# Optimization experiments

Hardware: AMD Instinct MI355X
Metric: run time of the kernel (lower is better)

The kernel has to match this reference:

```python
import jax, jax.numpy as jnp
import numpy as np

SEQ, B, CIN, H, K = 2048, 16, 512, 512, 2

def setup_inputs() -> dict:
    key = jax.random.key(0)
    k1, k2, k3 = jax.random.split(key, 3)
    x = jax.random.normal(k1, (SEQ, B, CIN), dtype=jnp.float32)
    W = jax.random.normal(k2, (3 * H, CIN, K), dtype=jnp.float32) * (1.0 / np.sqrt(CIN * K))
    b = jax.random.normal(k3, (3 * H,), dtype=jnp.float32) * 0.01
    return {"x": x, "W": W, "b": b}

def _qrnn_fo(x, W, b):
    # x: (T, B, Cin) -> conv input (B, Cin, T), causal left pad of K-1 zeros
    xb = jnp.transpose(x, (1, 2, 0))
    g = jax.lax.conv_general_dilated(
        xb, W, window_strides=(1,), padding=[(K - 1, 0)],
        dimension_numbers=("NCH", "OIH", "NCH"))
    g = g + b[None, :, None]
    g = jnp.transpose(g, (2, 0, 1))  # (T, B, 3H)
    zg, fg, og = jnp.split(g, 3, axis=-1)
    z = jnp.tanh(zg)
    f = jax.nn.sigmoid(fg)
    o = jax.nn.sigmoid(og)

    def step(c, gates_t):
        zt, ft, ot = gates_t
        c = ft * c + (1.0 - ft) * zt
        h = c * ot
        return c, h

    c0 = jnp.zeros((B, H), dtype=x.dtype)
    c_last, hs = jax.lax.scan(step, c0, (z, f, o))
    return hs, c_last

def reference(x, W, b):
    hs, c_last = _qrnn_fo(x, W, b)
    h_last = hs[-1]
    return hs, h_last[None, :], c_last[None, :]
```

## Files before the change

kernel.cpp:

```cpp
#include <hip/hip_runtime.h>

#define SEQ   2048
#define BATCH 16
#define CINCH 512
#define HDIM  512
#define NDIM  1536
#define TBM   (SEQ*BATCH)
#define KRED  1024
#define NCH   128
#define CHL   16
#define NCOL  8192

typedef unsigned short ushort_t;
typedef __bf16 bf16x8 __attribute__((ext_vector_type(8)));
typedef unsigned short u16x8 __attribute__((ext_vector_type(8)));
typedef float f32x4 __attribute__((ext_vector_type(4)));

__device__ __forceinline__ float bf2f(ushort_t u) {
    return __uint_as_float(((unsigned int)u) << 16);
}
__device__ __forceinline__ ushort_t f2bf(float x) {
    unsigned int u = __float_as_uint(x);
    unsigned int r = u + 0x7fffu + ((u >> 16) & 1u);
    return (ushort_t)(r >> 16);
}

#define CAST_BLK 8196
#define RPK_BLK  6144
__global__ void prep_kernel(const float* __restrict__ x, ushort_t* __restrict__ xb,
                            const float* __restrict__ W, ushort_t* __restrict__ wb) {
    if (blockIdx.x < CAST_BLK) {
        int e = (blockIdx.x * 256 + threadIdx.x) * 8;
        u16x8 r;
        if (e < BATCH * CINCH) {
            r = (u16x8){0, 0, 0, 0, 0, 0, 0, 0};
        } else {
            const float* p = x + (e - BATCH * CINCH);
            float4 v0 = *(const float4*)p;
            float4 v1 = *(const float4*)(p + 4);
            r[0] = f2bf(v0.x); r[1] = f2bf(v0.y); r[2] = f2bf(v0.z); r[3] = f2bf(v0.w);
            r[4] = f2bf(v1.x); r[5] = f2bf(v1.y); r[6] = f2bf(v1.z); r[7] = f2bf(v1.w);
        }
        *(u16x8*)(xb + e) = r;
    } else {
        int i = (blockIdx.x - CAST_BLK) * 256 + threadIdx.x;
        int o  = i >> 10;
        int r  = i & 1023;
        int k  = r >> 9;
        int ci = r & 511;
        wb[i] = f2bf(W[o * 1024 + ci * 2 + k]);
    }
}

__device__ __forceinline__ void load_lds_16B(const ushort_t* g, ushort_t* l) {
    auto* gp = reinterpret_cast<const __attribute__((address_space(1))) unsigned int*>(
        reinterpret_cast<uintptr_t>(g));
    auto* lp = reinterpret_cast<__attribute__((address_space(3))) unsigned int*>(
        reinterpret_cast<uintptr_t>(l));
    __builtin_amdgcn_global_load_lds(gp, lp, 16, 0, 0);
}

__global__ __launch_bounds__(256) void gemm_gates_kernel(
    const ushort_t* __restrict__ xb, const ushort_t* __restrict__ wb,
    const float* __restrict__ bias,
    ushort_t* __restrict__ zb, ushort_t* __restrict__ fb, ushort_t* __restrict__ ob) {

    __shared__ ushort_t smem[2 * 128 * 64];
    ushort_t* As = smem;
    ushort_t* Bs = smem + 128 * 64;

    const int tid  = threadIdx.x;
    const int w    = tid >> 6;
    const int lane = tid & 63;
    const int quad = lane >> 4;
    const int l15  = lane & 15;
    const int wm   = w & 1;
    const int wn   = w >> 1;
    const int nBase = blockIdx.x * 128;
    const int mBase = blockIdx.y * 128;

    const int srow = lane >> 3;
    const int scb  = lane & 7;

    f32x4 acc[4][4];
#pragma unroll
    for (int i = 0; i < 4; ++i)
#pragma unroll
        for (int j = 0; j < 4; ++j)
            acc[i][j] = (f32x4){0.f, 0.f, 0.f, 0.f};

    for (int kt = 0; kt < 16; ++kt) {
        __syncthreads();
        const long aOff = (kt < 8) ? (long)kt * 64 : (long)16 * 512 + (long)(kt - 8) * 64;
#pragma unroll
        for (int i = 0; i < 4; ++i) {
            const int row = w * 32 + i * 8 + srow;
            const int cbd = scb ^ (row & 7);
            const ushort_t* ga = xb + (long)(mBase + row) * 512 + aOff + cbd * 8;
            load_lds_16B(ga, &As[(w * 32 + i * 8) * 64]);
            const ushort_t* gb = wb + (long)(nBase + row) * 1024 + kt * 64 + cbd * 8;
            load_lds_16B(gb, &Bs[(w * 32 + i * 8) * 64]);
        }
        __syncthreads();

#pragma unroll
        for (int ks = 0; ks < 2; ++ks) {
            bf16x8 af[4], bfr[4];
            const int cbd = ks * 4 + quad;
#pragma unroll
            for (int mt = 0; mt < 4; ++mt) {
                int ml  = wm * 64 + mt * 16 + l15;
                int off = ml * 64 + ((cbd ^ (ml & 7)) * 8);
                af[mt] = __builtin_bit_cast(bf16x8, *(const u16x8*)(&As[off]));
            }
#pragma unroll
            for (int nt = 0; nt < 4; ++nt) {
                int nl  = wn * 64 + nt * 16 + l15;
                int off = nl * 64 + ((cbd ^ (nl & 7)) * 8);
                bfr[nt] = __builtin_bit_cast(bf16x8, *(const u16x8*)(&Bs[off]));
            }
#pragma unroll
            for (int mt = 0; mt < 4; ++mt)
#pragma unroll
                for (int nt = 0; nt < 4; ++nt)
                    acc[mt][nt] = __builtin_amdgcn_mfma_f32_16x16x32_bf16(
                        af[mt], bfr[nt], acc[mt][nt], 0, 0, 0);
        }
    }

    const int gate = nBase >> 9;
    const int hb   = nBase & 511;

    __syncthreads();
#pragma unroll
    for (int nt = 0; nt < 4; ++nt) {
        const int n_local = wn * 64 + nt * 16 + l15;
        const float bv = bias[nBase + n_local];
#pragma unroll
        for (int mt = 0; mt < 4; ++mt) {
#pragma unroll
            for (int r = 0; r < 4; ++r) {
                const int m_local = wm * 64 + mt * 16 + quad * 4 + r;
                float g = acc[mt][nt][r] + bv;
                float a;
                if (gate == 0) {
                    float e = __expf(-2.f * fabsf(g));
                    float t = (1.f - e) / (1.f + e);
                    a = copysignf(t, g);
                } else {
                    a = 1.f / (1.f + __expf(-g));
                }
                const int phys = ((n_local >> 3) ^ (m_local & 7)) * 8 + (n_local & 7);
                smem[m_local * 128 + phys] = f2bf(a);
            }
        }
    }
    __syncthreads();

    ushort_t* outp = (gate == 0) ? zb : (gate == 1) ? fb : ob;
#pragma unroll
    for (int s = 0; s < 8; ++s) {
        const int m_local = w * 32 + s * 4 + quad;
        const int blk = l15 ^ (m_local & 7);
        u16x8 v = *(const u16x8*)(&smem[m_local * 128 + blk * 8]);
        *(u16x8*)(outp + (long)(mBase + m_local) * 512 + hb + l15 * 8) = v;
    }
}

__global__ __launch_bounds__(256) void scan_compose(
    const ushort_t* __restrict__ zb, const ushort_t* __restrict__ fb,
    float* __restrict__ Acomp, float* __restrict__ Bcomp) {
    const int ch   = blockIdx.x >> 2;
    const int col0 = (((blockIdx.x & 3) * 256) + threadIdx.x) * 8;
    const long base = (long)ch * CHL * NCOL + col0;

    float A[8], Bv[8];
#pragma unroll
    for (int j = 0; j < 8; ++j) { A[j] = 1.f; Bv[j] = 0.f; }

    u16x8 zc = *(const u16x8*)(zb + base);
    u16x8 fc = *(const u16x8*)(fb + base);
    for (int t = 0; t < CHL; ++t) {
        u16x8 zn, fn;
        if (t + 1 < CHL) {
            zn = *(const u16x8*)(zb + base + (long)(t + 1) * NCOL);
            fn = *(const u16x8*)(fb + base + (long)(t + 1) * NCOL);
        }
#pragma unroll
        for (int j = 0; j < 8; ++j) {
            float f = bf2f(fc[j]), z = bf2f(zc[j]);
            Bv[j] = f * Bv[j] + (1.f - f) * z;
            A[j] *= f;
        }
        zc = zn; fc = fn;
    }
#pragma unroll
    for (int j = 0; j < 4; ++j) {
    }
    f32x4 a0 = {A[0], A[1], A[2], A[3]}, a1 = {A[4], A[5], A[6], A[7]};
    f32x4 b0 = {Bv[0], Bv[1], Bv[2], Bv[3]}, b1 = {Bv[4], Bv[5], Bv[6], Bv[7]};
    *(f32x4*)(Acomp + (long)ch * NCOL + col0)     = a0;
    *(f32x4*)(Acomp + (long)ch * NCOL + col0 + 4) = a1;
    *(f32x4*)(Bcomp + (long)ch * NCOL + col0)     = b0;
    *(f32x4*)(Bcomp + (long)ch * NCOL + col0 + 4) = b1;
}

__global__ void scan_prefix(const float* __restrict__ Acomp,
                            const float* __restrict__ Bcomp,
                            float* __restrict__ Cin) {
    const int col = blockIdx.x * 256 + threadIdx.x;
    float c = 0.f;
#pragma unroll 4
    for (int ch = 0; ch < NCH; ++ch) {
        Cin[ch * NCOL + col] = c;
        c = Acomp[ch * NCOL + col] * c + Bcomp[ch * NCOL + col];
    }
}

__global__ __launch_bounds__(256) void scan_apply(
    const ushort_t* __restrict__ zb, const ushort_t* __restrict__ fb,
    const ushort_t* __restrict__ ob, const float* __restrict__ Cin,
    float* __restrict__ out) {
    const int ch   = blockIdx.x >> 2;
    const int col0 = (((blockIdx.x & 3) * 256) + threadIdx.x) * 8;
    const long base = (long)ch * CHL * NCOL + col0;

    float c[8], h[8];
    f32x4 c0 = *(const f32x4*)(Cin + (long)ch * NCOL + col0);
    f32x4 c1 = *(const f32x4*)(Cin + (long)ch * NCOL + col0 + 4);
    c[0] = c0[0]; c[1] = c0[1]; c[2] = c0[2]; c[3] = c0[3];
    c[4] = c1[0]; c[5] = c1[1]; c[6] = c1[2]; c[7] = c1[3];

    u16x8 zc = *(const u16x8*)(zb + base);
    u16x8 fc = *(const u16x8*)(fb + base);
    u16x8 oc = *(const u16x8*)(ob + base);
    for (int t = 0; t < CHL; ++t) {
        u16x8 zn, fn, on;
        if (t + 1 < CHL) {
            zn = *(const u16x8*)(zb + base + (long)(t + 1) * NCOL);
            fn = *(const u16x8*)(fb + base + (long)(t + 1) * NCOL);
            on = *(const u16x8*)(ob + base + (long)(t + 1) * NCOL);
        }
#pragma unroll
        for (int j = 0; j < 8; ++j) {
            float f = bf2f(fc[j]), z = bf2f(zc[j]), o = bf2f(oc[j]);
            c[j] = f * c[j] + (1.f - f) * z;
            h[j] = c[j] * o;
        }
        f32x4 h0 = {h[0], h[1], h[2], h[3]}, h1 = {h[4], h[5], h[6], h[7]};
        *(f32x4*)(out + base + (long)t * NCOL)     = h0;
        *(f32x4*)(out + base + (long)t * NCOL + 4) = h1;
        zc = zn; fc = fn; oc = on;
    }
    if (ch == NCH - 1) {
        f32x4 h0 = {h[0], h[1], h[2], h[3]}, h1 = {h[4], h[5], h[6], h[7]};
        f32x4 cc0 = {c[0], c[1], c[2], c[3]}, cc1 = {c[4], c[5], c[6], c[7]};
        *(f32x4*)(out + (long)SEQ * NCOL + col0)            = h0;
        *(f32x4*)(out + (long)SEQ * NCOL + col0 + 4)        = h1;
        *(f32x4*)(out + (long)SEQ * NCOL + NCOL + col0)     = cc0;
        *(f32x4*)(out + (long)SEQ * NCOL + NCOL + col0 + 4) = cc1;
    }
}

extern "C" void kernel_launch(void* const* d_in, const int* in_sizes, int n_in,
                              void* d_out, int out_size, void* d_ws, size_t ws_size,
                              hipStream_t stream) {
    const float* x  = (const float*)d_in[0];
    const float* W  = (const float*)d_in[1];
    const float* bi = (const float*)d_in[2];
    float* out = (float*)d_out;

    char* ws = (char*)d_ws;
    const size_t xbN = (size_t)(TBM + BATCH) * CINCH;
    const size_t wbN = (size_t)NDIM * KRED;
    const size_t gN  = (size_t)TBM * HDIM;
    ushort_t* xb = (ushort_t*)ws;
    ushort_t* wb = (ushort_t*)(ws + xbN * 2);
    ushort_t* zb = (ushort_t*)(ws + xbN * 2 + wbN * 2);
    ushort_t* fb = zb + gN;
    ushort_t* ob = fb + gN;
    float* Acomp = (float*)ws;
    float* Bcomp = Acomp + NCH * NCOL;
    float* Cin   = Bcomp + NCH * NCOL;

    prep_kernel<<<CAST_BLK + RPK_BLK, 256, 0, stream>>>(x, xb, W, wb);
    dim3 ggrid(NDIM / 128, TBM / 128);
    gemm_gates_kernel<<<ggrid, 256, 0, stream>>>(xb, wb, bi, zb, fb, ob);
    scan_compose<<<NCH * 4, 256, 0, stream>>>(zb, fb, Acomp, Bcomp);
    scan_prefix<<<NCOL / 256, 256, 0, stream>>>(Acomp, Bcomp, Cin);
    scan_apply<<<NCH * 4, 256, 0, stream>>>(zb, fb, ob, Cin, out);
}
```

Baseline: 309.9 us.

## Shorten scan chunks, preload chunk gates, and swap GEMM grid rasterization

Halves the scan chunk length and doubles the chunk count, so the compose and apply kernels launch more blocks and each thread preloads all of its chunk's gate vectors before a fully unrolled recurrence. This is meant to expose more memory-level parallelism and occupancy in the scan kernels. The GEMM grid is transposed so consecutive blocks walk the M dimension rather than the N dimension, which changes which tiles share cache. In exchange, the serial prefix kernel now runs twice as many sequential steps, and the scratch buffers for the chunk summaries double in size.

New measurement: 308.2 us. Within noise of the previous version (-0.6%).

```diff
diff --git a/kernel.cpp b/kernel.cpp
--- a/kernel.cpp
+++ b/kernel.cpp
@@ -7,8 +7,8 @@
 #define NDIM  1536
 #define TBM   (SEQ*BATCH)
 #define KRED  1024
-#define NCH   128
-#define CHL   16
+#define NCH   256
+#define CHL   8
 #define NCOL  8192
 
 typedef unsigned short ushort_t;
@@ -76,8 +76,8 @@
     const int l15  = lane & 15;
     const int wm   = w & 1;
     const int wn   = w >> 1;
-    const int nBase = blockIdx.x * 128;
-    const int mBase = blockIdx.y * 128;
+    const int mBase = blockIdx.x * 128;
+    const int nBase = blockIdx.y * 128;
 
     const int srow = lane >> 3;
     const int scb  = lane & 7;
@@ -174,28 +174,23 @@
     const int col0 = (((blockIdx.x & 3) * 256) + threadIdx.x) * 8;
     const long base = (long)ch * CHL * NCOL + col0;
 
+    u16x8 zc[CHL], fc[CHL];
+#pragma unroll
+    for (int t = 0; t < CHL; ++t) {
+        zc[t] = *(const u16x8*)(zb + base + (long)t * NCOL);
+        fc[t] = *(const u16x8*)(fb + base + (long)t * NCOL);
+    }
     float A[8], Bv[8];
 #pragma unroll
     for (int j = 0; j < 8; ++j) { A[j] = 1.f; Bv[j] = 0.f; }
-
-    u16x8 zc = *(const u16x8*)(zb + base);
-    u16x8 fc = *(const u16x8*)(fb + base);
-    for (int t = 0; t < CHL; ++t) {
-        u16x8 zn, fn;
-        if (t + 1 < CHL) {
-            zn = *(const u16x8*)(zb + base + (long)(t + 1) * NCOL);
-            fn = *(const u16x8*)(fb + base + (long)(t + 1) * NCOL);
-        }
+#pragma unroll
+    for (int t = 0; t < CHL; ++t) {
 #pragma unroll
         for (int j = 0; j < 8; ++j) {
-            float f = bf2f(fc[j]), z = bf2f(zc[j]);
+            float f = bf2f(fc[t][j]), z = bf2f(zc[t][j]);
             Bv[j] = f * Bv[j] + (1.f - f) * z;
             A[j] *= f;
         }
-        zc = zn; fc = fn;
-    }
-#pragma unroll
-    for (int j = 0; j < 4; ++j) {
     }
     f32x4 a0 = {A[0], A[1], A[2], A[3]}, a1 = {A[4], A[5], A[6], A[7]};
     f32x4 b0 = {Bv[0], Bv[1], Bv[2], Bv[3]}, b1 = {Bv[4], Bv[5], Bv[6], Bv[7]};
@@ -210,7 +205,7 @@
                             float* __restrict__ Cin) {
     const int col = blockIdx.x * 256 + threadIdx.x;
     float c = 0.f;
-#pragma unroll 4
+#pragma unroll 8
     for (int ch = 0; ch < NCH; ++ch) {
         Cin[ch * NCOL + col] = c;
         c = Acomp[ch * NCOL + col] * c + Bcomp[ch * NCOL + col];
@@ -225,32 +220,30 @@
     const int col0 = (((blockIdx.x & 3) * 256) + threadIdx.x) * 8;
     const long base = (long)ch * CHL * NCOL + col0;
 
+    u16x8 zc[CHL], fc[CHL], oc[CHL];
+#pragma unroll
+    for (int t = 0; t < CHL; ++t) {
+        zc[t] = *(const u16x8*)(zb + base + (long)t * NCOL);
+        fc[t] = *(const u16x8*)(fb + base + (long)t * NCOL);
+        oc[t] = *(const u16x8*)(ob + base + (long)t * NCOL);
+    }
     float c[8], h[8];
     f32x4 c0 = *(const f32x4*)(Cin + (long)ch * NCOL + col0);
     f32x4 c1 = *(const f32x4*)(Cin + (long)ch * NCOL + col0 + 4);
     c[0] = c0[0]; c[1] = c0[1]; c[2] = c0[2]; c[3] = c0[3];
     c[4] = c1[0]; c[5] = c1[1]; c[6] = c1[2]; c[7] = c1[3];
 
-    u16x8 zc = *(const u16x8*)(zb + base);
-    u16x8 fc = *(const u16x8*)(fb + base);
-    u16x8 oc = *(const u16x8*)(ob + base);
-    for (int t = 0; t < CHL; ++t) {
-        u16x8 zn, fn, on;
-        if (t + 1 < CHL) {
-            zn = *(const u16x8*)(zb + base + (long)(t + 1) * NCOL);
-            fn = *(const u16x8*)(fb + base + (long)(t + 1) * NCOL);
-            on = *(const u16x8*)(ob + base + (long)(t + 1) * NCOL);
-        }
+#pragma unroll
+    for (int t = 0; t < CHL; ++t) {
 #pragma unroll
         for (int j = 0; j < 8; ++j) {
-            float f = bf2f(fc[j]), z = bf2f(zc[j]), o = bf2f(oc[j]);
+            float f = bf2f(fc[t][j]), z = bf2f(zc[t][j]), o = bf2f(oc[t][j]);
             c[j] = f * c[j] + (1.f - f) * z;
             h[j] = c[j] * o;
         }
         f32x4 h0 = {h[0], h[1], h[2], h[3]}, h1 = {h[4], h[5], h[6], h[7]};
         *(f32x4*)(out + base + (long)t * NCOL)     = h0;
         *(f32x4*)(out + base + (long)t * NCOL + 4) = h1;
-        zc = zn; fc = fn; oc = on;
     }
     if (ch == NCH - 1) {
         f32x4 h0 = {h[0], h[1], h[2], h[3]}, h1 = {h[4], h[5], h[6], h[7]};
@@ -284,7 +277,7 @@
     float* Cin   = Bcomp + NCH * NCOL;
 
     prep_kernel<<<CAST_BLK + RPK_BLK, 256, 0, stream>>>(x, xb, W, wb);
-    dim3 ggrid(NDIM / 128, TBM / 128);
+    dim3 ggrid(TBM / 128, NDIM / 128);
     gemm_gates_kernel<<<ggrid, 256, 0, stream>>>(xb, wb, bi, zb, fb, ob);
     scan_compose<<<NCH * 4, 256, 0, stream>>>(zb, fb, Acomp, Bcomp);
     scan_prefix<<<NCOL / 256, 256, 0, stream>>>(Acomp, Bcomp, Cin);
```
